# Kernel optimization log

Hardware: AMD Instinct MI355X
Metric: run time of the kernel (lower is better)

## Reference

```python
import jax, jax.numpy as jnp
import numpy as np

TAU = 1.0
TOP_P = 0.9
EPS = 1e-5


def _nucleus_adj(X, W1, W2, W3):
    h = jnp.tanh(X @ W1.T)            # [N, d_attn]
    q = h @ W2.T                      # [N, d_attn]
    k = X @ W3.T                      # [N, d_attn]
    scores = (q @ k.T) / TAU          # [N, N]
    probs = jax.nn.softmax(scores, axis=-1)
    # nucleus (top-p): keep smallest prefix of desc-sorted probs covering mass p
    order = jnp.argsort(-probs, axis=-1)
    sp = jnp.take_along_axis(probs, order, axis=-1)
    cs = jnp.cumsum(sp, axis=-1)
    keep_sorted = (cs - sp) < TOP_P   # keep tokens before mass exceeds p (incl. crossing one)
    inv = jnp.argsort(order, axis=-1)
    keep = jnp.take_along_axis(keep_sorted, inv, axis=-1)
    A = jnp.where(keep, probs, 0.0)
    return A / jnp.sum(A, axis=-1, keepdims=True)


def _sequence_priors(N, dtype):
    # forward/backward chain priors (S=None case): row-stochastic shift matrices
    Rf = jnp.eye(N, k=-1, dtype=dtype).at[0, 0].set(1.0)
    Rb = jnp.eye(N, k=1, dtype=dtype).at[N - 1, N - 1].set(1.0)
    return Rf, Rb


def setup_inputs() -> dict:
    key = jax.random.key(0)
    ks = jax.random.split(key, 8)
    N, d_in, d_attn, steps = 4096, 512, 64, 2
    s = 0.02
    return {
        "X": jax.random.normal(ks[0], (N, d_in), jnp.float32),
        "W1": jax.random.normal(ks[1], (d_attn, d_in), jnp.float32) * s,
        "W2": jax.random.normal(ks[2], (d_attn, d_attn), jnp.float32) * s,
        "W3": jax.random.normal(ks[3], (d_attn, d_in), jnp.float32) * s,
        "U1": jax.random.normal(ks[4], (steps, d_in, d_in), jnp.float32) * s,
        "U2": jax.random.normal(ks[5], (steps, d_in, d_in), jnp.float32) * s,
        "U3": jax.random.normal(ks[6], (steps, d_in, d_in), jnp.float32) * s,
        "gamma": jnp.ones((d_in,), jnp.float32),
        "beta": jnp.zeros((d_in,), jnp.float32),
    }


def reference(X, W1, W2, W3, U1, U2, U3, gamma, beta):
    N = X.shape[0]
    steps = U1.shape[0]
    Rf, Rb = _sequence_priors(N, X.dtype)
    Z = jnp.zeros_like(X)
    Xf, Xb, Xa = X, X, X
    for n in range(steps):
        A = _nucleus_adj(Xa, W1, W2, W3)
        Xf = Rf @ Xf
        Xb = Rb @ Xb
        Xa = A @ Xa
        P = Xf @ U1[n].T + Xb @ U2[n].T
        F = Xa @ U3[n].T
        Z = Z + (P + F)  # dropout is identity in eval mode
    y = X + Z
    mu = jnp.mean(y, axis=-1, keepdims=True)
    var = jnp.var(y, axis=-1, keepdims=True)
    return (y - mu) * jax.lax.rsqrt(var + EPS) * gamma + beta
```

## Files before the change

### kernel.cpp

```cpp
#include <hip/hip_runtime.h>
#include <hip/hip_bf16.h>
#include <math.h>

typedef short bf16x8 __attribute__((ext_vector_type(8)));
typedef float f32x4 __attribute__((ext_vector_type(4)));
typedef unsigned short u16;
typedef unsigned long long u64;

#define N_TOK  4096
#define D_IN   512
#define D_ATTN 64
#define NBI    1024
#define CAPW   128
#define TOPP   0.9f
#define LN_EPS 1e-5f
#define AMAXV  (N_TOK - 1)
#define FLTMAX 3.402823466e38f
#define MSCALE 524288.0f

__device__ __forceinline__ u16 f2bf(float f) {
  unsigned int u = __float_as_uint(f);
  return (u16)((u + 0x7FFFu + ((u >> 16) & 1u)) >> 16);
}

__device__ __forceinline__ float bf2f(u16 v) {
  return __uint_as_float(((unsigned)v) << 16);
}

__device__ __forceinline__ unsigned mfix(float e) {
  return (unsigned)(e * MSCALE + 0.5f);
}

__device__ __forceinline__ void gload16(const u16* g, u16* l) {
  __builtin_amdgcn_global_load_lds(
      (const __attribute__((address_space(1))) unsigned int*)g,
      (__attribute__((address_space(3))) unsigned int*)l, 16, 0, 0);
}

template<int EPI, int NSEG, int KSEG>
__global__ __launch_bounds__(256)
void gemm128(const u16* __restrict__ A0, int lda0, int sh0, const u16* __restrict__ B0, int ldb0,
             const u16* __restrict__ A1, int lda1, int sh1, const u16* __restrict__ B1, int ldb1,
             const u16* __restrict__ A2, int lda2, int sh2, const u16* __restrict__ B2, int ldb2,
             float* __restrict__ Cf, u16* __restrict__ Cb, u16* __restrict__ CbT,
             int ldc, int ldct)
{
  constexpr int BN = 64;
  constexpr int NF = BN / 32;
  constexpr int IPSEG = KSEG >> 6;
  constexpr int TOTAL = NSEG * IPSEG;
  constexpr int DB = (TOTAL < 3) ? TOTAL : 3;

  __shared__ u16 sA[DB][128 * 64];
  __shared__ u16 sB[DB][BN * 64];

  const int tid  = threadIdx.x;
  const int wave = tid >> 6;
  const int lane = tid & 63;
  const int l15  = lane & 15;
  const int l4   = lane >> 4;
  const int brow = blockIdx.y << 7;
  const int bcol = blockIdx.x * BN;
  const int kz   = blockIdx.z * KSEG;
  const int wr64 = (wave >> 1) << 6;
  const int wcol = (wave & 1) * (BN >> 1);

  auto stage = [&](int buf, int it) {
    int seg = (NSEG == 1) ? 0 : (it / IPSEG);
    int kk  = (NSEG == 1) ? (it << 6) : ((it % IPSEG) << 6);
    const u16 *Ab, *Bb; int la, lb, sh;
    if (seg == 0)      { Ab = A0; la = lda0; sh = sh0; Bb = B0; lb = ldb0; }
    else if (seg == 1) { Ab = A1; la = lda1; sh = sh1; Bb = B1; lb = ldb1; }
    else               { Ab = A2; la = lda2; sh = sh2; Bb = B2; lb = ldb2; }
    kk += kz;
#pragma unroll
    for (int q = 0; q < 4; ++q) {
      int idx = q * 256 + tid;
      int row = idx >> 3;
      int chunk = (idx & 7) ^ (row & 7);
      int r = brow + row + sh;
      r = (r < 0) ? 0 : ((r > AMAXV) ? AMAXV : r);
      gload16(Ab + (size_t)r * la + kk + chunk * 8, &sA[buf][idx * 8]);
    }
#pragma unroll
    for (int q = 0; q < BN / 32; ++q) {
      int idx = q * 256 + tid;
      int row = idx >> 3;
      int chunk = (idx & 7) ^ (row & 7);
      gload16(Bb + (size_t)(bcol + row) * lb + kk + chunk * 8, &sB[buf][idx * 8]);
    }
  };

  f32x4 acc[4][NF];
#pragma unroll
  for (int m = 0; m < 4; ++m)
#pragma unroll
    for (int n = 0; n < NF; ++n) {
      acc[m][n][0] = 0.f; acc[m][n][1] = 0.f; acc[m][n][2] = 0.f; acc[m][n][3] = 0.f;
    }

  stage(0, 0);
  if (TOTAL > 1) stage(1 % DB, 1);

  for (int i = 0; i < TOTAL; ++i) {
    if (i + 1 < TOTAL) asm volatile("s_waitcnt vmcnt(6)" ::: "memory");
    else               asm volatile("s_waitcnt vmcnt(0)" ::: "memory");
    __builtin_amdgcn_s_barrier();
    if (i + 2 < TOTAL) stage((i + 2) % DB, i + 2);
    const int c = i % DB;
#pragma unroll
    for (int ks = 0; ks < 2; ++ks) {
      bf16x8 af[4], bfr[NF];
#pragma unroll
      for (int m = 0; m < 4; ++m) {
        int ar = wr64 + m * 16 + l15;
        af[m] = *(const bf16x8*)&sA[c][ar * 64 + (((ks << 2) + l4) ^ (ar & 7)) * 8];
      }
#pragma unroll
      for (int n = 0; n < NF; ++n) {
        int br = wcol + n * 16 + l15;
        bfr[n] = *(const bf16x8*)&sB[c][br * 64 + (((ks << 2) + l4) ^ (br & 7)) * 8];
      }
#pragma unroll
      for (int m = 0; m < 4; ++m)
#pragma unroll
        for (int n = 0; n < NF; ++n)
          acc[m][n] = __builtin_amdgcn_mfma_f32_16x16x32_bf16(af[m], bfr[n], acc[m][n], 0, 0, 0);
    }
  }

  float* Cfz = (EPI == 6 || EPI == 3) ? (Cf + (size_t)blockIdx.z * (size_t)ldct) : Cf;
#pragma unroll
  for (int m = 0; m < 4; ++m)
#pragma unroll
    for (int n = 0; n < NF; ++n)
#pragma unroll
      for (int r = 0; r < 4; ++r) {
        const int row = brow + wr64 + m * 16 + l4 * 4 + r;
        const int col = bcol + wcol + n * 16 + l15;
        const float v = acc[m][n][r];
        if (EPI == 0) Cf[(size_t)row * ldc + col] = v;
        if (EPI == 1) Cb[(size_t)row * ldc + col] = f2bf(tanhf(v));
        if (EPI == 2) Cb[(size_t)row * ldc + col] = f2bf(v);
        if (EPI == 3) Cfz[(size_t)row * ldc + col] += v;
        if (EPI == 4) {
          u16 hv = f2bf(v);
          Cb [(size_t)row * ldc  + col] = hv;
          CbT[(size_t)col * ldct + row] = hv;
        }
        if (EPI == 5) {
          if (col < 64) Cb [(size_t)row * 64 + col]        = f2bf(tanhf(v));
          else          CbT[(size_t)row * 64 + (col - 64)] = f2bf(v);
        }
        if (EPI == 6) Cfz[(size_t)row * ldc + col] = v;
      }
}

__global__ __launch_bounds__(256)
void pvfix(const float* __restrict__ Zp, u16* __restrict__ Xa, u16* __restrict__ XaT)
{
  const size_t st = (size_t)N_TOK * D_IN;
  __shared__ u16 tile[64][65];
  const int bx = blockIdx.x, by = blockIdx.y;
  const int t = threadIdx.x;
  const int tx = t & 15, ty = t >> 4;
#pragma unroll
  for (int i = 0; i < 4; ++i) {
    int r = by * 64 + ty + 16 * i;
    int c = bx * 64 + tx * 4;
    size_t idx = (size_t)r * D_IN + c;
    float4 a = *(const float4*)&Zp[idx];
    float4 b = *(const float4*)&Zp[idx + st];
    float4 d = *(const float4*)&Zp[idx + 2 * st];
    float4 e = *(const float4*)&Zp[idx + 3 * st];
    u16 q0 = f2bf(a.x + b.x + d.x + e.x), q1 = f2bf(a.y + b.y + d.y + e.y);
    u16 q2 = f2bf(a.z + b.z + d.z + e.z), q3 = f2bf(a.w + b.w + d.w + e.w);
    *(ushort4*)&Xa[idx] = make_ushort4(q0, q1, q2, q3);
    tile[ty + 16 * i][tx * 4 + 0] = q0;
    tile[ty + 16 * i][tx * 4 + 1] = q1;
    tile[ty + 16 * i][tx * 4 + 2] = q2;
    tile[ty + 16 * i][tx * 4 + 3] = q3;
  }
  __syncthreads();
#pragma unroll
  for (int i = 0; i < 4; ++i) {
    int cc = ty + 16 * i;
    int rq = tx * 4;
    u16 o0 = tile[rq + 0][cc], o1 = tile[rq + 1][cc];
    u16 o2 = tile[rq + 2][cc], o3 = tile[rq + 3][cc];
    *(ushort4*)&XaT[(size_t)(bx * 64 + cc) * N_TOK + by * 64 + rq] =
        make_ushort4(o0, o1, o2, o3);
  }
}

__global__ __launch_bounds__(256)
void nucleus_block(const u16* __restrict__ S, u16* __restrict__ A, int apitch)
{
  const int t = threadIdx.x;
  const int wv = t >> 6, ln = t & 63;

  __shared__ unsigned hist[4][NBI];
  __shared__ float ge[CAPW];
  __shared__ int   gcol[CAPW];
  __shared__ unsigned gm[CAPW];
  __shared__ unsigned char kf[CAPW];
  __shared__ float sMin[4], sMax[4], sDen[4];
  __shared__ int   sCnt[4], sS[4];
  __shared__ unsigned sScan[4];
  __shared__ unsigned s_Ab;
  __shared__ int   s_cnt;

  for (int rr = 0; rr < 2; ++rr) {
    const int row = blockIdx.x + rr * (N_TOK / 2);
    const u16* srow = S + (size_t)row * N_TOK;
    u16* arow = A + (size_t)row * apitch;

    __syncthreads();

    float evf[16];
    float lmax = -FLTMAX, lmin = FLTMAX;
#pragma unroll
    for (int q = 0; q < 4; ++q) {
      ushort4 v = ((const ushort4*)srow)[q * 256 + t];
      float e0 = bf2f(v.x), e1 = bf2f(v.y), e2 = bf2f(v.z), e3 = bf2f(v.w);
      evf[4*q+0] = e0; evf[4*q+1] = e1; evf[4*q+2] = e2; evf[4*q+3] = e3;
      lmax = fmaxf(lmax, fmaxf(fmaxf(e0, e1), fmaxf(e2, e3)));
      lmin = fminf(lmin, fminf(fminf(e0, e1), fminf(e2, e3)));
    }
#pragma unroll
    for (int o = 32; o; o >>= 1) {
      lmax = fmaxf(lmax, __shfl_xor(lmax, o));
      lmin = fminf(lmin, __shfl_xor(lmin, o));
    }
    if (ln == 0) { sMax[wv] = lmax; sMin[wv] = lmin; }
    __syncthreads();
    const float smax = fmaxf(fmaxf(sMax[0], sMax[1]), fmaxf(sMax[2], sMax[3]));
    const float smin = fminf(fminf(sMin[0], sMin[1]), fminf(sMin[2], sMin[3]));

#pragma unroll
    for (int j = 0; j < 16; ++j) evf[j] = __expf(evf[j] - smax);

    unsigned keepM = 0, cand = 0xFFFFu;
    unsigned Agt = 0, T = 0;
    bool haveT = false;
    float lo = __expf(smin - smax);
    float width = fmaxf(1.0f - lo, 1e-30f);

    for (int lev = 0; lev < 12; ++lev) {
      __syncthreads();
      {
        uint4 z; z.x = 0; z.y = 0; z.z = 0; z.w = 0;
        ((uint4*)hist[0])[t] = z; ((uint4*)hist[1])[t] = z;
        ((uint4*)hist[2])[t] = z; ((uint4*)hist[3])[t] = z;
      }
      int myCnt = __popc(cand);
      float cmin = FLTMAX, cmax = -FLTMAX;
#pragma unroll
      for (int j = 0; j < 16; ++j)
        if ((cand >> j) & 1) { float e = evf[j]; cmin = fminf(cmin, e); cmax = fmaxf(cmax, e); }
      int ct = myCnt;
#pragma unroll
      for (int o = 32; o; o >>= 1) {
        ct   += __shfl_xor(ct, o);
        cmin  = fminf(cmin, __shfl_xor(cmin, o));
        cmax  = fmaxf(cmax, __shfl_xor(cmax, o));
      }
      if (ln == 0) { sCnt[wv] = ct; sMin[wv] = cmin; sMax[wv] = cmax; }
      __syncthreads();
      const int tot = sCnt[0] + sCnt[1] + sCnt[2] + sCnt[3];
      cmin = fminf(fminf(sMin[0], sMin[1]), fminf(sMin[2], sMin[3]));
      cmax = fmaxf(fmaxf(sMax[0], sMax[1]), fmaxf(sMax[2], sMax[3]));

      if (tot == 0) break;

      if (haveT && (cmin == cmax || lev == 11)) {
        const float v = cmax;
        const unsigned mv = mfix(v);
        int r;
        if (T <= Agt) r = 0;
        else if (mv == 0) r = tot;
        else { unsigned need = T - Agt; r = (int)((need + mv - 1) / mv); if (r > tot) r = tot; }
        int cq[4], excl[4];
#pragma unroll
        for (int q = 0; q < 4; ++q) {
          cq[q] = __popc((cand >> (4 * q)) & 0xF);
          int sc = cq[q];
#pragma unroll
          for (int o = 1; o < 64; o <<= 1) { int u = __shfl_up(sc, o); if (ln >= o) sc += u; }
          excl[q] = sc - cq[q];
          if (ln == 63) hist[wv][NBI - 4 + q] = (unsigned)(excl[q] + cq[q]);
        }
        __syncthreads();
        int qtot[4], woffq[4];
#pragma unroll
        for (int q = 0; q < 4; ++q) {
          unsigned w0 = hist[0][NBI - 4 + q], w1 = hist[1][NBI - 4 + q],
                   w2 = hist[2][NBI - 4 + q], w3 = hist[3][NBI - 4 + q];
          woffq[q] = (wv > 0 ? (int)w0 : 0) + (wv > 1 ? (int)w1 : 0) + (wv > 2 ? (int)w2 : 0);
          qtot[q]  = (int)(w0 + w1 + w2 + w3);
        }
        int qbase = 0;
#pragma unroll
        for (int q = 0; q < 4; ++q) {
          int seen = 0;
#pragma unroll
          for (int jj = 0; jj < 4; ++jj) {
            int j = 4 * q + jj;
            if ((cand >> j) & 1) {
              int rank = qbase + woffq[q] + excl[q] + seen;
              if (rank < r) keepM |= 1u << j;
              ++seen;
            }
          }
          qbase += qtot[q];
        }
        break;
      }

      if (haveT && tot <= CAPW) {
        if (t == 0) s_cnt = 0;
        __syncthreads();
#pragma unroll
        for (int j = 0; j < 16; ++j) {
          if ((cand >> j) & 1) {
            int i = atomicAdd(&s_cnt, 1);
            ge[i] = evf[j];
            gm[i] = mfix(evf[j]);
            gcol[i] = ((j >> 2) << 10) + (t << 2) + (j & 3);
          }
        }
        __syncthreads();
        const int cnt = s_cnt;
        if (t < cnt) {
          float ei = ge[t]; int ci = gcol[t];
          unsigned m = Agt;
          for (int u = 0; u < cnt; ++u) {
            float el = ge[u];
            if (el > ei || (el == ei && gcol[u] < ci)) m += gm[u];
          }
          kf[t] = (m < T) ? 1 : 0;
        }
        __syncthreads();
        for (int u = 0; u < cnt; ++u) {
          int c = gcol[u];
          if (((c >> 2) & 255) == t && kf[u])
            keepM |= 1u << (((c >> 10) << 2) | (c & 3));
        }
        break;
      }

      const float scale = (float)NBI / width;
      __syncthreads();
      unsigned* Hw = hist[wv];
#pragma unroll
      for (int j = 0; j < 16; ++j) {
        if ((cand >> j) & 1) {
          float e = evf[j];
          int b = (int)((e - lo) * scale);
          b = (b < 0) ? 0 : ((b > NBI - 1) ? NBI - 1 : b);
          atomicAdd(&Hw[b], mfix(e));
        }
      }
      __syncthreads();
      unsigned hv[4];
      {
        uint4 a0 = ((const uint4*)hist[0])[t];
        uint4 a1 = ((const uint4*)hist[1])[t];
        uint4 a2 = ((const uint4*)hist[2])[t];
        uint4 a3 = ((const uint4*)hist[3])[t];
        hv[0] = a0.x + a1.x + a2.x + a3.x;
        hv[1] = a0.y + a1.y + a2.y + a3.y;
        hv[2] = a0.z + a1.z + a2.z + a3.z;
        hv[3] = a0.w + a1.w + a2.w + a3.w;
      }
      unsigned sl = (hv[0] + hv[1]) + (hv[2] + hv[3]);
      unsigned pv = sl;
#pragma unroll
      for (int o = 1; o < 64; o <<= 1) { unsigned u = __shfl_up(pv, o); if (ln >= o) pv += u; }
      if (ln == 63) sScan[wv] = pv;
      __syncthreads();
      const unsigned woff = (wv > 0 ? sScan[0] : 0u) + (wv > 1 ? sScan[1] : 0u) + (wv > 2 ? sScan[2] : 0u);
      const unsigned CM   = sScan[0] + sScan[1] + sScan[2] + sScan[3];
      if (!haveT) {
        T = (unsigned)((9ULL * (unsigned long long)CM) / 10ULL);
        haveT = true;
      }
      const unsigned incl = pv + woff;
      unsigned Arun = Agt + (CM - incl);
      int lb = -1; unsigned Ab = 0;
#pragma unroll
      for (int j = 3; j >= 0; --j) {
        unsigned bm = hv[j];
        if (Arun < T && Arun + bm >= T) { lb = j; Ab = Arun; }
        Arun += bm;
      }
      int bl = (lb >= 0) ? ((t << 2) | lb) : -1;
      int s = bl;
#pragma unroll
      for (int o = 32; o; o >>= 1) s = max(s, __shfl_xor(s, o));
      if (ln == 0) sS[wv] = s;
      __syncthreads();
      s = max(max(sS[0], sS[1]), max(sS[2], sS[3]));
      if (s < 0) { keepM |= cand; break; }
      if (bl == s) s_Ab = Ab;
      __syncthreads();
      const unsigned Abnd = s_Ab;
      unsigned nk = 0, nc = 0;
#pragma unroll
      for (int j = 0; j < 16; ++j) {
        if ((cand >> j) & 1) {
          float e = evf[j];
          int b = (int)((e - lo) * scale);
          b = (b < 0) ? 0 : ((b > NBI - 1) ? NBI - 1 : b);
          if (b > s) nk |= 1u << j;
          else if (b == s) nc |= 1u << j;
        }
      }
      keepM |= nk;
      cand = nc;
      Agt = Abnd;
      width = fmaxf(width * (1.0f / NBI), 1e-37f);
      lo = lo + (float)s * width;
    }

    float dl = 0.f;
#pragma unroll
    for (int j = 0; j < 16; ++j)
      if ((keepM >> j) & 1) dl += evf[j];
#pragma unroll
    for (int o = 32; o; o >>= 1) dl += __shfl_xor(dl, o);
    if (ln == 0) sDen[wv] = dl;
    __syncthreads();
    float den = sDen[0] + sDen[1] + sDen[2] + sDen[3];
    if (den <= 0.f) den = 1.f;
    const float invd = 1.0f / den;

#pragma unroll
    for (int q = 0; q < 4; ++q) {
      u16 rr4[4];
#pragma unroll
      for (int j = 0; j < 4; ++j) {
        int b = 4 * q + j;
        float val = ((keepM >> b) & 1) ? evf[b] * invd : 0.f;
        rr4[j] = f2bf(val);
      }
      ((ushort4*)arow)[q * 256 + t] = make_ushort4(rr4[0], rr4[1], rr4[2], rr4[3]);
    }
  }
}

__global__ void cvt_all(const float* __restrict__ X,  const float* __restrict__ W1,
                        const float* __restrict__ W3, const float* __restrict__ W2,
                        const float* __restrict__ U1, const float* __restrict__ U2,
                        const float* __restrict__ U3,
                        u16* __restrict__ Xbf, u16* __restrict__ Xa0,
                        u16* __restrict__ W13b, u16* __restrict__ W2b,
                        u16* __restrict__ U1b, u16* __restrict__ U2b, u16* __restrict__ U3b)
{
  const int NX = 524288, NW = 8192, NW2 = 1024, NU = 131072;
  const int TOT = NX + 2 * NW + NW2 + 3 * NU;
  const int stride = gridDim.x * 256;
  for (int i = blockIdx.x * 256 + threadIdx.x; i < TOT; i += stride) {
    const float* s; u16* d; int rel; bool dual = false;
    if (i < NX)                       { s = X;  d = Xbf;  rel = i; dual = true; }
    else if (i < NX + NW)             { s = W1; d = W13b; rel = i - NX; }
    else if (i < NX + 2*NW)           { s = W3; d = W13b + (size_t)4*NW; rel = i - NX - NW; }
    else if (i < NX + 2*NW + NW2)     { s = W2; d = W2b;  rel = i - NX - 2*NW; }
    else if (i < NX + 2*NW + NW2 + NU){ s = U1; d = U1b;  rel = i - NX - 2*NW - NW2; }
    else if (i < NX + 2*NW + NW2+2*NU){ s = U2; d = U2b;  rel = i - NX - 2*NW - NW2 - NU; }
    else                              { s = U3; d = U3b;  rel = i - NX - 2*NW - NW2 - 2*NU; }
    float4 v = ((const float4*)s)[rel];
    ushort4 o;
    o.x = f2bf(v.x); o.y = f2bf(v.y); o.z = f2bf(v.z); o.w = f2bf(v.w);
    ((ushort4*)d)[rel] = o;
    if (dual) ((ushort4*)Xa0)[rel] = o;
  }
}

__global__ __launch_bounds__(256)
void tpose_bf(const float* __restrict__ X, u16* __restrict__ XT)
{
  __shared__ u16 tile[32][33];
  const int bc = blockIdx.x * 32;
  const int br = blockIdx.y * 32;
  const int tx = threadIdx.x & 31, ty = threadIdx.x >> 5;
#pragma unroll
  for (int i = 0; i < 32; i += 8)
    tile[ty + i][tx] = f2bf(X[(size_t)(br + ty + i) * D_IN + bc + tx]);
  __syncthreads();
#pragma unroll
  for (int i = 0; i < 32; i += 8)
    XT[(size_t)(bc + ty + i) * N_TOK + br + tx] = tile[tx][ty + i];
}

__global__ __launch_bounds__(256)
void ln_kernel(const float* __restrict__ X, const float* __restrict__ Z0,
               const float* __restrict__ Z1, float* __restrict__ OUT,
               const float* __restrict__ gamma, const float* __restrict__ beta)
{
  const int tid = threadIdx.x;
  __shared__ float red[4];
  __shared__ float s_mu, s_var;
  for (int rr = 0; rr < 2; ++rr) {
    const int row = blockIdx.x + rr * (N_TOK / 2);
    const size_t base = (size_t)row * D_IN;
    __syncthreads();
    float y0 = X[base + tid] + Z0[base + tid];
    float y1 = X[base + tid + 256] + Z0[base + tid + 256];
    if (Z1) { y0 += Z1[base + tid]; y1 += Z1[base + tid + 256]; }
    float s = y0 + y1;
    for (int o = 32; o; o >>= 1) s += __shfl_xor(s, o);
    if ((tid & 63) == 0) red[tid >> 6] = s;
    __syncthreads();
    if (tid == 0) s_mu = (red[0] + red[1] + red[2] + red[3]) * (1.f / D_IN);
    __syncthreads();
    const float mu = s_mu;
    float d0 = y0 - mu, d1 = y1 - mu;
    float v = d0 * d0 + d1 * d1;
    for (int o = 32; o; o >>= 1) v += __shfl_xor(v, o);
    if ((tid & 63) == 0) red[tid >> 6] = v;
    __syncthreads();
    if (tid == 0) s_var = (red[0] + red[1] + red[2] + red[3]) * (1.f / D_IN);
    __syncthreads();
    const float rs = rsqrtf(s_var + LN_EPS);
    OUT[base + tid]       = d0 * rs * gamma[tid]       + beta[tid];
    OUT[base + tid + 256] = d1 * rs * gamma[tid + 256] + beta[tid + 256];
  }
}

extern "C" void kernel_launch(void* const* d_in, const int* in_sizes, int n_in,
                              void* d_out, int out_size, void* d_ws, size_t ws_size,
                              hipStream_t stream)
{
  const float* X     = (const float*)d_in[0];
  const float* W1    = (const float*)d_in[1];
  const float* W2    = (const float*)d_in[2];
  const float* W3    = (const float*)d_in[3];
  const float* U1    = (const float*)d_in[4];
  const float* U2    = (const float*)d_in[5];
  const float* U3    = (const float*)d_in[6];
  const float* gamma = (const float*)d_in[7];
  const float* beta  = (const float*)d_in[8];

  char* w = (char*)d_ws;
  u16* S16    = (u16*)w;              w += (size_t)N_TOK * N_TOK * 2;
  u16* Xbf    = (u16*)w;              w += (size_t)N_TOK * D_IN * 2;
  u16* Xa0    = (u16*)w;              w += (size_t)N_TOK * D_IN * 2;
  u16* Xa1    = (u16*)w;              w += (size_t)N_TOK * D_IN * 2;
  u16* XaT0   = (u16*)w;              w += (size_t)D_IN * N_TOK * 2;
  u16* XaT1   = (u16*)w;              w += (size_t)D_IN * N_TOK * 2;
  u16* hb     = (u16*)w;              w += (size_t)N_TOK * D_ATTN * 2;
  u16* qb     = (u16*)w;              w += (size_t)N_TOK * D_ATTN * 2;
  u16* kb     = (u16*)w;              w += (size_t)N_TOK * D_ATTN * 2;
  u16* W13b   = (u16*)w;              w += (size_t)2 * D_ATTN * D_IN * 2;
  u16* W2b    = (u16*)w;              w += (size_t)D_ATTN * D_ATTN * 2;
  u16* U1b    = (u16*)w;              w += (size_t)2 * D_IN * D_IN * 2;
  u16* U2b    = (u16*)w;              w += (size_t)2 * D_IN * D_IN * 2;
  u16* U3b    = (u16*)w;              w += (size_t)2 * D_IN * D_IN * 2;

  size_t used = (size_t)(w - (char*)d_ws);
  u16* Abuf;
  int  apitch = N_TOK;
  if (ws_size >= used + (size_t)N_TOK * N_TOK * 2) {
    Abuf = (u16*)w;
    w += (size_t)N_TOK * N_TOK * 2;
  } else {
    Abuf = S16;
  }
  used = (size_t)(w - (char*)d_ws);
  float* Zp = nullptr;
  const bool splitK = (ws_size >= used + 4 * (size_t)N_TOK * D_IN * 4);
  if (splitK) { Zp = (float*)w; w += 4 * (size_t)N_TOK * D_IN * 4; }
  used = (size_t)(w - (char*)d_ws);
  float* Zq = nullptr;
  const bool projSplit = (ws_size >= used + 2 * (size_t)N_TOK * D_IN * 4);
  if (projSplit) { Zq = (float*)w; w += 2 * (size_t)N_TOK * D_IN * 4; }

  float* Z = (float*)d_out;

  if (projSplit) {
    hipMemsetAsync(Zq, 0, 2 * (size_t)N_TOK * D_IN * 4, stream);
  } else {
    hipMemsetAsync(d_out, 0, (size_t)N_TOK * D_IN * 4, stream);
  }

  cvt_all<<<1024, 256, 0, stream>>>(X, W1, W3, W2, U1, U2, U3,
                                    Xbf, Xa0, W13b, W2b, U1b, U2b, U3b);
  tpose_bf<<<dim3(D_IN / 32, N_TOK / 32), 256, 0, stream>>>(X, XaT0);

  u16* XaC[2]  = {Xa0, Xa1};
  u16* XaTC[2] = {XaT0, XaT1};

  for (int n = 0; n < 2; ++n) {
    const int cur = n & 1, nxt = cur ^ 1;
    const size_t uoff = (size_t)n * D_IN * D_IN;
    gemm128<5, 1, D_IN><<<dim3(2, 32), 256, 0, stream>>>(
        XaC[cur], D_IN, 0, W13b, D_IN,
        nullptr, 0, 0, nullptr, 0, nullptr, 0, 0, nullptr, 0,
        nullptr, hb, kb, 64, 64);
    gemm128<2, 1, D_ATTN><<<dim3(1, 32), 256, 0, stream>>>(
        hb, D_ATTN, 0, W2b, D_ATTN,
        nullptr, 0, 0, nullptr, 0, nullptr, 0, 0, nullptr, 0,
        nullptr, qb, nullptr, D_ATTN, 0);
    gemm128<2, 1, D_ATTN><<<dim3(64, 32), 256, 0, stream>>>(
        qb, D_ATTN, 0, kb, D_ATTN,
        nullptr, 0, 0, nullptr, 0, nullptr, 0, 0, nullptr, 0,
        nullptr, S16, nullptr, N_TOK, 0);
    nucleus_block<<<N_TOK / 2, 256, 0, stream>>>(S16, Abuf, apitch);
    if (splitK) {
      gemm128<6, 1, N_TOK / 4><<<dim3(8, 32, 4), 256, 0, stream>>>(
          Abuf, apitch, 0, XaTC[cur], N_TOK,
          nullptr, 0, 0, nullptr, 0, nullptr, 0, 0, nullptr, 0,
          Zp, nullptr, nullptr, D_IN, N_TOK * D_IN);
      pvfix<<<dim3(D_IN / 64, N_TOK / 64), 256, 0, stream>>>(
          Zp, XaC[nxt], XaTC[nxt]);
    } else {
      gemm128<4, 1, N_TOK><<<dim3(8, 32), 256, 0, stream>>>(
          Abuf, apitch, 0, XaTC[cur], N_TOK,
          nullptr, 0, 0, nullptr, 0, nullptr, 0, 0, nullptr, 0,
          nullptr, XaC[nxt], XaTC[nxt], D_IN, N_TOK);
    }
    if (projSplit) {
      gemm128<3, 3, D_IN / 2><<<dim3(8, 32, 2), 256, 0, stream>>>(
          Xbf, D_IN, -(n + 1), U1b + uoff, D_IN,
          Xbf, D_IN,  (n + 1), U2b + uoff, D_IN,
          XaC[nxt], D_IN, 0,   U3b + uoff, D_IN,
          Zq, nullptr, nullptr, D_IN, N_TOK * D_IN);
    } else {
      gemm128<3, 3, D_IN><<<dim3(8, 32), 256, 0, stream>>>(
          Xbf, D_IN, -(n + 1), U1b + uoff, D_IN,
          Xbf, D_IN,  (n + 1), U2b + uoff, D_IN,
          XaC[nxt], D_IN, 0,   U3b + uoff, D_IN,
          Z, nullptr, nullptr, D_IN, 0);
    }
  }

  if (projSplit) {
    ln_kernel<<<N_TOK / 2, 256, 0, stream>>>(
        X, Zq, Zq + (size_t)N_TOK * D_IN, (float*)d_out, gamma, beta);
  } else {
    ln_kernel<<<N_TOK / 2, 256, 0, stream>>>(
        X, Z, nullptr, (float*)d_out, gamma, beta);
  }
}
```

Baseline: 337.3 us.

## Hoist shift-prior projections into one upfront GEMM and trim redundant work

The forward and backward shift-chain projections for both steps are now computed by a single 4-segment GEMM before the loop, so the per-step projection GEMM only handles the attention path. The last pvfix skips writing the transposed Xa, which is no longer needed. The GEMM gains a configurable pipeline depth (DBMAX=2 for several calls, cutting LDS use). The nucleus selection loop is reordered so the first level skips the candidate reduction and barrier. The changes are meant to cut launches, redundant transposes and shared-memory pressure, at the cost of shallower prefetch in some GEMMs.

```diff
diff --git a/kernel.cpp b/kernel.cpp
--- a/kernel.cpp
+++ b/kernel.cpp
@@ -37,11 +37,12 @@
       (__attribute__((address_space(3))) unsigned int*)l, 16, 0, 0);
 }
 
-template<int EPI, int NSEG, int KSEG>
+template<int EPI, int NSEG, int KSEG, int DBMAX = 3>
 __global__ __launch_bounds__(256)
 void gemm128(const u16* __restrict__ A0, int lda0, int sh0, const u16* __restrict__ B0, int ldb0,
              const u16* __restrict__ A1, int lda1, int sh1, const u16* __restrict__ B1, int ldb1,
              const u16* __restrict__ A2, int lda2, int sh2, const u16* __restrict__ B2, int ldb2,
+             const u16* __restrict__ A3, int lda3, int sh3, const u16* __restrict__ B3, int ldb3,
              float* __restrict__ Cf, u16* __restrict__ Cb, u16* __restrict__ CbT,
              int ldc, int ldct)
 {
@@ -49,7 +50,8 @@
   constexpr int NF = BN / 32;
   constexpr int IPSEG = KSEG >> 6;
   constexpr int TOTAL = NSEG * IPSEG;
-  constexpr int DB = (TOTAL < 3) ? TOTAL : 3;
+  constexpr int DB = (TOTAL < DBMAX) ? TOTAL : DBMAX;
+  constexpr int DEPTH = (DB > 1) ? (DB - 1) : 0;
 
   __shared__ u16 sA[DB][128 * 64];
   __shared__ u16 sB[DB][BN * 64];
@@ -71,7 +73,8 @@
     const u16 *Ab, *Bb; int la, lb, sh;
     if (seg == 0)      { Ab = A0; la = lda0; sh = sh0; Bb = B0; lb = ldb0; }
     else if (seg == 1) { Ab = A1; la = lda1; sh = sh1; Bb = B1; lb = ldb1; }
-    else               { Ab = A2; la = lda2; sh = sh2; Bb = B2; lb = ldb2; }
+    else if (seg == 2) { Ab = A2; la = lda2; sh = sh2; Bb = B2; lb = ldb2; }
+    else               { Ab = A3; la = lda3; sh = sh3; Bb = B3; lb = ldb3; }
     kk += kz;
 #pragma unroll
     for (int q = 0; q < 4; ++q) {
@@ -100,13 +103,13 @@
     }
 
   stage(0, 0);
-  if (TOTAL > 1) stage(1 % DB, 1);
+  if (DEPTH >= 2 && TOTAL > 1) stage(1 % DB, 1);
 
   for (int i = 0; i < TOTAL; ++i) {
-    if (i + 1 < TOTAL) asm volatile("s_waitcnt vmcnt(6)" ::: "memory");
-    else               asm volatile("s_waitcnt vmcnt(0)" ::: "memory");
+    if (DEPTH >= 2 && i + 1 < TOTAL) asm volatile("s_waitcnt vmcnt(6)" ::: "memory");
+    else                             asm volatile("s_waitcnt vmcnt(0)" ::: "memory");
     __builtin_amdgcn_s_barrier();
-    if (i + 2 < TOTAL) stage((i + 2) % DB, i + 2);
+    if (DEPTH > 0 && i + DEPTH < TOTAL) stage((i + DEPTH) % DB, i + DEPTH);
     const int c = i % DB;
 #pragma unroll
     for (int ks = 0; ks < 2; ++ks) {
@@ -156,6 +159,7 @@
       }
 }
 
+template<bool WRT>
 __global__ __launch_bounds__(256)
 void pvfix(const float* __restrict__ Zp, u16* __restrict__ Xa, u16* __restrict__ XaT)
 {
@@ -176,20 +180,24 @@
     u16 q0 = f2bf(a.x + b.x + d.x + e.x), q1 = f2bf(a.y + b.y + d.y + e.y);
     u16 q2 = f2bf(a.z + b.z + d.z + e.z), q3 = f2bf(a.w + b.w + d.w + e.w);
     *(ushort4*)&Xa[idx] = make_ushort4(q0, q1, q2, q3);
-    tile[ty + 16 * i][tx * 4 + 0] = q0;
-    tile[ty + 16 * i][tx * 4 + 1] = q1;
-    tile[ty + 16 * i][tx * 4 + 2] = q2;
-    tile[ty + 16 * i][tx * 4 + 3] = q3;
-  }
-  __syncthreads();
-#pragma unroll
-  for (int i = 0; i < 4; ++i) {
-    int cc = ty + 16 * i;
-    int rq = tx * 4;
-    u16 o0 = tile[rq + 0][cc], o1 = tile[rq + 1][cc];
-    u16 o2 = tile[rq + 2][cc], o3 = tile[rq + 3][cc];
-    *(ushort4*)&XaT[(size_t)(bx * 64 + cc) * N_TOK + by * 64 + rq] =
-        make_ushort4(o0, o1, o2, o3);
+    if (WRT) {
+      tile[ty + 16 * i][tx * 4 + 0] = q0;
+      tile[ty + 16 * i][tx * 4 + 1] = q1;
+      tile[ty + 16 * i][tx * 4 + 2] = q2;
+      tile[ty + 16 * i][tx * 4 + 3] = q3;
+    }
+  }
+  if (WRT) {
+    __syncthreads();
+#pragma unroll
+    for (int i = 0; i < 4; ++i) {
+      int cc = ty + 16 * i;
+      int rq = tx * 4;
+      u16 o0 = tile[rq + 0][cc], o1 = tile[rq + 1][cc];
+      u16 o2 = tile[rq + 2][cc], o3 = tile[rq + 3][cc];
+      *(ushort4*)&XaT[(size_t)(bx * 64 + cc) * N_TOK + by * 64 + rq] =
+          make_ushort4(o0, o1, o2, o3);
+    }
   }
 }
 
@@ -247,109 +255,110 @@
     float width = fmaxf(1.0f - lo, 1e-30f);
 
     for (int lev = 0; lev < 12; ++lev) {
-      __syncthreads();
+      if (lev > 0) {
+        int myCnt = __popc(cand);
+        float cmin = FLTMAX, cmax = -FLTMAX;
+#pragma unroll
+        for (int j = 0; j < 16; ++j)
+          if ((cand >> j) & 1) { float e = evf[j]; cmin = fminf(cmin, e); cmax = fmaxf(cmax, e); }
+        int ct = myCnt;
+#pragma unroll
+        for (int o = 32; o; o >>= 1) {
+          ct   += __shfl_xor(ct, o);
+          cmin  = fminf(cmin, __shfl_xor(cmin, o));
+          cmax  = fmaxf(cmax, __shfl_xor(cmax, o));
+        }
+        if (ln == 0) { sCnt[wv] = ct; sMin[wv] = cmin; sMax[wv] = cmax; }
+        __syncthreads();
+        const int tot = sCnt[0] + sCnt[1] + sCnt[2] + sCnt[3];
+        cmin = fminf(fminf(sMin[0], sMin[1]), fminf(sMin[2], sMin[3]));
+        cmax = fmaxf(fmaxf(sMax[0], sMax[1]), fmaxf(sMax[2], sMax[3]));
+
+        if (tot == 0) break;
+
+        if (cmin == cmax || lev == 11) {
+          const float v = cmax;
+          const unsigned mv = mfix(v);
+          int r;
+          if (T <= Agt) r = 0;
+          else if (mv == 0) r = tot;
+          else { unsigned need = T - Agt; r = (int)((need + mv - 1) / mv); if (r > tot) r = tot; }
+          int cq[4], excl[4];
+#pragma unroll
+          for (int q = 0; q < 4; ++q) {
+            cq[q] = __popc((cand >> (4 * q)) & 0xF);
+            int sc = cq[q];
+#pragma unroll
+            for (int o = 1; o < 64; o <<= 1) { int u = __shfl_up(sc, o); if (ln >= o) sc += u; }
+            excl[q] = sc - cq[q];
+            if (ln == 63) hist[wv][NBI - 4 + q] = (unsigned)(excl[q] + cq[q]);
+          }
+          __syncthreads();
+          int qtot[4], woffq[4];
+#pragma unroll
+          for (int q = 0; q < 4; ++q) {
+            unsigned w0 = hist[0][NBI - 4 + q], w1 = hist[1][NBI - 4 + q],
+                     w2 = hist[2][NBI - 4 + q], w3 = hist[3][NBI - 4 + q];
+            woffq[q] = (wv > 0 ? (int)w0 : 0) + (wv > 1 ? (int)w1 : 0) + (wv > 2 ? (int)w2 : 0);
+            qtot[q]  = (int)(w0 + w1 + w2 + w3);
+          }
+          int qbase = 0;
+#pragma unroll
+          for (int q = 0; q < 4; ++q) {
+            int seen = 0;
+#pragma unroll
+            for (int jj = 0; jj < 4; ++jj) {
+              int j = 4 * q + jj;
+              if ((cand >> j) & 1) {
+                int rank = qbase + woffq[q] + excl[q] + seen;
+                if (rank < r) keepM |= 1u << j;
+                ++seen;
+              }
+            }
+            qbase += qtot[q];
+          }
+          break;
+        }
+
+        if (tot <= CAPW) {
+          if (t == 0) s_cnt = 0;
+          __syncthreads();
+#pragma unroll
+          for (int j = 0; j < 16; ++j) {
+            if ((cand >> j) & 1) {
+              int i = atomicAdd(&s_cnt, 1);
+              ge[i] = evf[j];
+              gm[i] = mfix(evf[j]);
+              gcol[i] = ((j >> 2) << 10) + (t << 2) + (j & 3);
+            }
+          }
+          __syncthreads();
+          const int cnt = s_cnt;
+          if (t < cnt) {
+            float ei = ge[t]; int ci = gcol[t];
+            unsigned m = Agt;
+            for (int u = 0; u < cnt; ++u) {
+              float el = ge[u];
+              if (el > ei || (el == ei && gcol[u] < ci)) m += gm[u];
+            }
+            kf[t] = (m < T) ? 1 : 0;
+          }
+          __syncthreads();
+          for (int u = 0; u < cnt; ++u) {
+            int c = gcol[u];
+            if (((c >> 2) & 255) == t && kf[u])
+              keepM |= 1u << (((c >> 10) << 2) | (c & 3));
+          }
+          break;
+        }
+      }
+
+      const float scale = (float)NBI / width;
       {
         uint4 z; z.x = 0; z.y = 0; z.z = 0; z.w = 0;
         ((uint4*)hist[0])[t] = z; ((uint4*)hist[1])[t] = z;
         ((uint4*)hist[2])[t] = z; ((uint4*)hist[3])[t] = z;
       }
-      int myCnt = __popc(cand);
-      float cmin = FLTMAX, cmax = -FLTMAX;
-#pragma unroll
-      for (int j = 0; j < 16; ++j)
-        if ((cand >> j) & 1) { float e = evf[j]; cmin = fminf(cmin, e); cmax = fmaxf(cmax, e); }
-      int ct = myCnt;
-#pragma unroll
-      for (int o = 32; o; o >>= 1) {
-        ct   += __shfl_xor(ct, o);
-        cmin  = fminf(cmin, __shfl_xor(cmin, o));
-        cmax  = fmaxf(cmax, __shfl_xor(cmax, o));
-      }
-      if (ln == 0) { sCnt[wv] = ct; sMin[wv] = cmin; sMax[wv] = cmax; }
-      __syncthreads();
-      const int tot = sCnt[0] + sCnt[1] + sCnt[2] + sCnt[3];
-      cmin = fminf(fminf(sMin[0], sMin[1]), fminf(sMin[2], sMin[3]));
-      cmax = fmaxf(fmaxf(sMax[0], sMax[1]), fmaxf(sMax[2], sMax[3]));
-
-      if (tot == 0) break;
-
-      if (haveT && (cmin == cmax || lev == 11)) {
-        const float v = cmax;
-        const unsigned mv = mfix(v);
-        int r;
-        if (T <= Agt) r = 0;
-        else if (mv == 0) r = tot;
-        else { unsigned need = T - Agt; r = (int)((need + mv - 1) / mv); if (r > tot) r = tot; }
-        int cq[4], excl[4];
-#pragma unroll
-        for (int q = 0; q < 4; ++q) {
-          cq[q] = __popc((cand >> (4 * q)) & 0xF);
-          int sc = cq[q];
-#pragma unroll
-          for (int o = 1; o < 64; o <<= 1) { int u = __shfl_up(sc, o); if (ln >= o) sc += u; }
-          excl[q] = sc - cq[q];
-          if (ln == 63) hist[wv][NBI - 4 + q] = (unsigned)(excl[q] + cq[q]);
-        }
-        __syncthreads();
-        int qtot[4], woffq[4];
-#pragma unroll
-        for (int q = 0; q < 4; ++q) {
-          unsigned w0 = hist[0][NBI - 4 + q], w1 = hist[1][NBI - 4 + q],
-                   w2 = hist[2][NBI - 4 + q], w3 = hist[3][NBI - 4 + q];
-          woffq[q] = (wv > 0 ? (int)w0 : 0) + (wv > 1 ? (int)w1 : 0) + (wv > 2 ? (int)w2 : 0);
-          qtot[q]  = (int)(w0 + w1 + w2 + w3);
-        }
-        int qbase = 0;
-#pragma unroll
-        for (int q = 0; q < 4; ++q) {
-          int seen = 0;
-#pragma unroll
-          for (int jj = 0; jj < 4; ++jj) {
-            int j = 4 * q + jj;
-            if ((cand >> j) & 1) {
-              int rank = qbase + woffq[q] + excl[q] + seen;
-              if (rank < r) keepM |= 1u << j;
-              ++seen;
-            }
-          }
-          qbase += qtot[q];
-        }
-        break;
-      }
-
-      if (haveT && tot <= CAPW) {
-        if (t == 0) s_cnt = 0;
-        __syncthreads();
-#pragma unroll
-        for (int j = 0; j < 16; ++j) {
-          if ((cand >> j) & 1) {
-            int i = atomicAdd(&s_cnt, 1);
-            ge[i] = evf[j];
-            gm[i] = mfix(evf[j]);
-            gcol[i] = ((j >> 2) << 10) + (t << 2) + (j & 3);
-          }
-        }
-        __syncthreads();
-        const int cnt = s_cnt;
-        if (t < cnt) {
-          float ei = ge[t]; int ci = gcol[t];
-          unsigned m = Agt;
-          for (int u = 0; u < cnt; ++u) {
-            float el = ge[u];
-            if (el > ei || (el == ei && gcol[u] < ci)) m += gm[u];
-          }
-          kf[t] = (m < T) ? 1 : 0;
-        }
-        __syncthreads();
-        for (int u = 0; u < cnt; ++u) {
-          int c = gcol[u];
-          if (((c >> 2) & 255) == t && kf[u])
-            keepM |= 1u << (((c >> 10) << 2) | (c & 3));
-        }
-        break;
-      }
-
-      const float scale = (float)NBI / width;
       __syncthreads();
       unsigned* Hw = hist[wv];
 #pragma unroll
@@ -542,6 +551,8 @@
   const float* gamma = (const float*)d_in[7];
   const float* beta  = (const float*)d_in[8];
 
+#define NILSEG nullptr, 0, 0, nullptr, 0
+
   char* w = (char*)d_ws;
   u16* S16    = (u16*)w;              w += (size_t)N_TOK * N_TOK * 2;
   u16* Xbf    = (u16*)w;              w += (size_t)N_TOK * D_IN * 2;
@@ -588,49 +599,64 @@
                                     Xbf, Xa0, W13b, W2b, U1b, U2b, U3b);
   tpose_bf<<<dim3(D_IN / 32, N_TOK / 32), 256, 0, stream>>>(X, XaT0);
 
+  const size_t UST = (size_t)D_IN * D_IN;
+
+  if (projSplit) {
+    gemm128<3, 4, D_IN / 2, 2><<<dim3(8, 32, 2), 256, 0, stream>>>(
+        Xbf, D_IN, -1, U1b, D_IN,
+        Xbf, D_IN, +1, U2b, D_IN,
+        Xbf, D_IN, -2, U1b + UST, D_IN,
+        Xbf, D_IN, +2, U2b + UST, D_IN,
+        Zq, nullptr, nullptr, D_IN, N_TOK * D_IN);
+  }
+
   u16* XaC[2]  = {Xa0, Xa1};
   u16* XaTC[2] = {XaT0, XaT1};
 
   for (int n = 0; n < 2; ++n) {
     const int cur = n & 1, nxt = cur ^ 1;
-    const size_t uoff = (size_t)n * D_IN * D_IN;
+    const size_t uoff = (size_t)n * UST;
     gemm128<5, 1, D_IN><<<dim3(2, 32), 256, 0, stream>>>(
         XaC[cur], D_IN, 0, W13b, D_IN,
-        nullptr, 0, 0, nullptr, 0, nullptr, 0, 0, nullptr, 0,
+        NILSEG, NILSEG, NILSEG,
         nullptr, hb, kb, 64, 64);
     gemm128<2, 1, D_ATTN><<<dim3(1, 32), 256, 0, stream>>>(
         hb, D_ATTN, 0, W2b, D_ATTN,
-        nullptr, 0, 0, nullptr, 0, nullptr, 0, 0, nullptr, 0,
+        NILSEG, NILSEG, NILSEG,
         nullptr, qb, nullptr, D_ATTN, 0);
     gemm128<2, 1, D_ATTN><<<dim3(64, 32), 256, 0, stream>>>(
         qb, D_ATTN, 0, kb, D_ATTN,
-        nullptr, 0, 0, nullptr, 0, nullptr, 0, 0, nullptr, 0,
+        NILSEG, NILSEG, NILSEG,
         nullptr, S16, nullptr, N_TOK, 0);
     nucleus_block<<<N_TOK / 2, 256, 0, stream>>>(S16, Abuf, apitch);
     if (splitK) {
-      gemm128<6, 1, N_TOK / 4><<<dim3(8, 32, 4), 256, 0, stream>>>(
+      gemm128<6, 1, N_TOK / 4, 2><<<dim3(8, 32, 4), 256, 0, stream>>>(
           Abuf, apitch, 0, XaTC[cur], N_TOK,
-          nullptr, 0, 0, nullptr, 0, nullptr, 0, 0, nullptr, 0,
+          NILSEG, NILSEG, NILSEG,
           Zp, nullptr, nullptr, D_IN, N_TOK * D_IN);
-      pvfix<<<dim3(D_IN / 64, N_TOK / 64), 256, 0, stream>>>(
-          Zp, XaC[nxt], XaTC[nxt]);
+      if (n == 0)
+        pvfix<true><<<dim3(D_IN / 64, N_TOK / 64), 256, 0, stream>>>(
+            Zp, XaC[nxt], XaTC[nxt]);
+      else
+        pvfix<false><<<dim3(D_IN / 64, N_TOK / 64), 256, 0, stream>>>(
+            Zp, XaC[nxt], nullptr);
     } else {
       gemm128<4, 1, N_TOK><<<dim3(8, 32), 256, 0, stream>>>(
           Abuf, apitch, 0, XaTC[cur], N_TOK,
-          nullptr, 0, 0, nullptr, 0, nullptr, 0, 0, nullptr, 0,
+          NILSEG, NILSEG, NILSEG,
           nullptr, XaC[nxt], XaTC[nxt], D_IN, N_TOK);
     }
     if (projSplit) {
-      gemm128<3, 3, D_IN / 2><<<dim3(8, 32, 2), 256, 0, stream>>>(
-          Xbf, D_IN, -(n + 1), U1b + uoff, D_IN,
-          Xbf, D_IN,  (n + 1), U2b + uoff, D_IN,
-          XaC[nxt], D_IN, 0,   U3b + uoff, D_IN,
+      gemm128<3, 1, D_IN / 2, 2><<<dim3(8, 32, 2), 256, 0, stream>>>(
+          XaC[nxt], D_IN, 0, U3b + uoff, D_IN,
+          NILSEG, NILSEG, NILSEG,
           Zq, nullptr, nullptr, D_IN, N_TOK * D_IN);
     } else {
       gemm128<3, 3, D_IN><<<dim3(8, 32), 256, 0, stream>>>(
           Xbf, D_IN, -(n + 1), U1b + uoff, D_IN,
           Xbf, D_IN,  (n + 1), U2b + uoff, D_IN,
           XaC[nxt], D_IN, 0,   U3b + uoff, D_IN,
+          NILSEG,
           Z, nullptr, nullptr, D_IN, 0);
     }
   }
```

Result: slower. 360.3 us (+6.8%).
